# Kernel optimization log

Hardware: AMD Instinct MI355X
Metric: run time of the kernel (lower is better)

Reference implementation:

```python
import jax, jax.numpy as jnp
import numpy as np

B_TREES, NARY, HS, NHEAD, NLVL = 16, 3, 512, 2, 6
EDIM = 352
LN_EPS = 1e-5

def _build_structure():
    # forest of B_TREES perfect ternary trees, depth NLVL; nodes numbered leaves-first, level-major
    off, o = {}, 0
    for l in range(NLVL - 1, -1, -1):
        off[l] = o
        o += B_TREES * 3 ** l
    node_ids = [off[l] + np.arange(B_TREES * 3 ** l) for l in range(NLVL)]
    child_idx = {}
    for l in range(NLVL - 1):
        m = 3 ** l
        t = np.repeat(np.arange(B_TREES), m)
        p = np.tile(np.arange(m), B_TREES)
        base = off[l + 1] + t * (3 ** (l + 1)) + 3 * p
        child_idx[l] = base[:, None] + np.arange(NARY)[None, :]
    return o, node_ids, child_idx

N_NODES, NODE_IDS, CHILD_IDX = _build_structure()

def _ln(x, w, b):
    mu = x.mean(-1, keepdims=True)
    var = x.var(-1, keepdims=True)
    return (x - mu) / jnp.sqrt(var + LN_EPS) * w + b

def _mha(x, wqkv, bqkv, wo, bo):
    # x: [S, B, H]; torch MHA with batch_first=False (seq dim 0, as in reduce_func)
    S, B, H = x.shape
    hd = H // NHEAD
    q, k, v = jnp.split(x @ wqkv.T + bqkv, 3, axis=-1)
    q = q.reshape(S, B, NHEAD, hd)
    k = k.reshape(S, B, NHEAD, hd)
    v = v.reshape(S, B, NHEAD, hd)
    scores = jnp.einsum('sbnd,tbnd->bnst', q, k) / jnp.sqrt(jnp.asarray(hd, x.dtype))
    attn = jax.nn.softmax(scores, axis=-1)
    o = jnp.einsum('bnst,tbnd->sbnd', attn, v).reshape(S, B, H)
    return o @ wo.T + bo

def _transformer(x, qkv_w, qkv_b, out_w, out_b, ln1_w, ln1_b, ff1_w, ff1_b, ff2_w, ff2_b, ln2_w, ln2_b):
    # 2 post-norm TransformerEncoderLayers, relu FF, dropout off (eval)
    for i in range(2):
        x = _ln(x + _mha(x, qkv_w[i], qkv_b[i], out_w[i], out_b[i]), ln1_w[i], ln1_b[i])
        ff = jax.nn.relu(x @ ff1_w[i].T + ff1_b[i]) @ ff2_w[i].T + ff2_b[i]
        x = _ln(x + ff, ln2_w[i], ln2_b[i])
    return x

def _forward(floats, ints):
    (user_emb, poi_emb, cat_emb, coo_emb, time_pos, W_iou, U_iou, b_iou,
     W_f, U_f, b_f, qkv_w, qkv_b, out_w, out_b, ln1_w, ln1_b, ff1_w, ff1_b,
     ff2_w, ff2_b, ln2_w, ln2_b, dec_poi_w, dec_poi_b, dec_cat_w, dec_cat_b,
     dec_coo_w, dec_coo_b) = floats
    user_ids, poi_ids, cat_ids, coo_ids, time_ids, mask = ints
    mi = mask.astype(jnp.int32)
    x = jnp.concatenate([user_emb[user_ids * mi], poi_emb[poi_ids * mi],
                         cat_emb[cat_ids * mi], coo_emb[coo_ids * mi]], axis=1)
    x = x + 0.5 * time_pos[time_ids * mi]
    x = x * mask.astype(x.dtype)[:, None]  # embed_dropout is identity in eval; per-node mask
    h = jnp.zeros((N_NODES, HS), x.dtype)
    c = jnp.zeros((N_NODES, HS), x.dtype)
    # leaves: reduce never fires -> iou stays at W_iou(x) (no b_iou), c = 0
    leaf = NODE_IDS[NLVL - 1]
    i0, o0, u0 = jnp.split(x[leaf] @ W_iou.T, 3, axis=1)
    c_leaf = jax.nn.sigmoid(i0) * jnp.tanh(u0)
    h = h.at[leaf].set(jax.nn.sigmoid(o0) * jnp.tanh(c_leaf))
    c = c.at[leaf].set(c_leaf)
    # topological propagation, bottom-up level frontiers
    for l in range(NLVL - 2, -1, -1):
        idx = NODE_IDS[l]
        ci = CHILD_IDX[l]
        m = idx.shape[0]
        h_ch = h[ci]  # mailbox gather [m, nary, HS]
        c_ch = c[ci]
        xl = x[idx]
        Wx = jnp.tile(xl @ W_f.T, (1, NARY))
        f = jax.nn.sigmoid(Wx + h_ch.reshape(m, NARY * HS) @ U_f.T + jnp.tile(b_f, (1, NARY)))
        h_att = _transformer(h_ch, qkv_w, qkv_b, out_w, out_b, ln1_w, ln1_b,
                             ff1_w, ff1_b, ff2_w, ff2_b, ln2_w, ln2_b)
        iou = xl @ W_iou.T + h_att.reshape(m, NARY * HS) @ U_iou.T + b_iou
        c_red = jnp.sum(f.reshape(m, NARY, HS) * c_ch, axis=1)
        i1, o1, u1 = jnp.split(iou, 3, axis=1)
        c_new = jax.nn.sigmoid(i1) * jnp.tanh(u1) + c_red
        h_new = jax.nn.sigmoid(o1) * jnp.tanh(c_new)
        h = h.at[idx].set(h_new)
        c = c.at[idx].set(c_new)
    # model_dropout identity in eval
    y_poi = h @ dec_poi_w.T + dec_poi_b
    y_cat = h @ dec_cat_w.T + dec_cat_b
    y_coo = h @ dec_coo_w.T + dec_coo_b
    return y_poi, y_cat, y_coo

def setup_inputs():
    key = jax.random.key(0)
    ks = iter(jax.random.split(key, 64))
    def rn(shape, s=0.05):
        return jax.random.normal(next(ks), shape, dtype=jnp.float32) * s
    def ri(shape, hi):
        return jax.random.randint(next(ks), shape, 0, hi, dtype=jnp.int32)
    N = N_NODES
    return dict(
        user_ids=ri([N], 3000), poi_ids=ri([N], 5000), cat_ids=ri([N], 300),
        coo_ids=ri([N], 1024), time_ids=ri([N], 96), mask=ri([N], 2),
        user_emb=rn([3000, 128], 0.02), poi_emb=rn([5000, 128], 0.02),
        cat_emb=rn([300, 32], 0.02), coo_emb=rn([1024, 64], 0.02),
        time_pos=rn([96, EDIM], 0.02),
        W_iou=rn([3 * HS, EDIM]), U_iou=rn([3 * HS, NARY * HS]), b_iou=jnp.zeros((1, 3 * HS)),
        W_f=rn([HS, EDIM]), U_f=rn([NARY * HS, NARY * HS]), b_f=jnp.zeros((1, HS)),
        qkv_w=rn([2, 3 * HS, HS]), qkv_b=jnp.zeros((2, 3 * HS)),
        out_w=rn([2, HS, HS]), out_b=jnp.zeros((2, HS)),
        ln1_w=jnp.ones((2, HS)), ln1_b=jnp.zeros((2, HS)),
        ff1_w=rn([2, HS, HS]), ff1_b=jnp.zeros((2, HS)),
        ff2_w=rn([2, HS, HS]), ff2_b=jnp.zeros((2, HS)),
        ln2_w=jnp.ones((2, HS)), ln2_b=jnp.zeros((2, HS)),
        dec_poi_w=rn([5000, HS]), dec_poi_b=jnp.zeros((5000,)),
        dec_cat_w=rn([300, HS]), dec_cat_b=jnp.zeros((300,)),
        dec_coo_w=rn([1024, HS]), dec_coo_b=jnp.zeros((1024,)),
    )

def reference(user_ids, poi_ids, cat_ids, coo_ids, time_ids, mask,
              user_emb, poi_emb, cat_emb, coo_emb, time_pos,
              W_iou, U_iou, b_iou, W_f, U_f, b_f,
              qkv_w, qkv_b, out_w, out_b, ln1_w, ln1_b, ff1_w, ff1_b,
              ff2_w, ff2_b, ln2_w, ln2_b,
              dec_poi_w, dec_poi_b, dec_cat_w, dec_cat_b, dec_coo_w, dec_coo_b):
    floats = (user_emb, poi_emb, cat_emb, coo_emb, time_pos, W_iou, U_iou, b_iou,
              W_f, U_f, b_f, qkv_w, qkv_b, out_w, out_b, ln1_w, ln1_b, ff1_w, ff1_b,
              ff2_w, ff2_b, ln2_w, ln2_b, dec_poi_w, dec_poi_b, dec_cat_w, dec_cat_b,
              dec_coo_w, dec_coo_b)
    ints = (user_ids, poi_ids, cat_ids, coo_ids, time_ids, mask)
    return _forward(floats, ints)
```

## Files before the change

kernel.cpp:

```cpp
#include <hip/hip_runtime.h>
#include <hip/hip_bf16.h>


namespace {

constexpr int NN = 5824;
constexpr int ED = 352;

typedef __bf16 bf16;
typedef short s16x8 __attribute__((ext_vector_type(8)));
typedef float f32x4 __attribute__((ext_vector_type(4)));

__device__ __forceinline__ float sigmoidf_(float x) { return 1.f / (1.f + expf(-x)); }

__device__ __forceinline__ void gload_lds16(const void* g, void* s) {
  __builtin_amdgcn_global_load_lds(
      (const __attribute__((address_space(1))) unsigned int*)g,
      (__attribute__((address_space(3))) unsigned int*)s, 16, 0, 0);
}

template <int MODE, bool DUAL, bool BPAIR, bool BF32>
__global__ __launch_bounds__(256) void bgemm_k(
    const bf16* __restrict__ A, const bf16* __restrict__ Alo,
    const bf16* __restrict__ Bh_, const bf16* __restrict__ Bl_,
    const float* __restrict__ Bf0, const float* __restrict__ Bf1,
    const float* __restrict__ Bf2,
    void* __restrict__ Cp, bf16* __restrict__ Clo, const float* __restrict__ Cacc,
    const float* __restrict__ bias, const float* __restrict__ bias1,
    const float* __restrict__ bias2, bf16* __restrict__ VTout, int mpad,
    int M, int N, int K, int lda, int ldb, int ldc, float alpha,
    long long sA1, long long sA2, long long sB1, long long sB2,
    long long sC1, long long sC2, int nh) {
  const int bz = blockIdx.z;
  const int b1 = bz / nh, b2 = bz - b1 * nh;
  A += (long long)b1 * sA1 + (long long)b2 * sA2;
  if (DUAL) Alo += (long long)b1 * sA1 + (long long)b2 * sA2;
  if (!BF32) {
    Bh_ += (long long)b1 * sB1 + (long long)b2 * sB2;
    if (BPAIR) Bl_ += (long long)b1 * sB1 + (long long)b2 * sB2;
  }
  const long long coff = (long long)b1 * sC1 + (long long)b2 * sC2;
  const int bm = blockIdx.y * 128, bn = blockIdx.x * 128;
  __shared__ bf16 As[128 * 32];
  __shared__ bf16 Ls[DUAL ? 128 * 32 : 8];
  __shared__ bf16 Bh[128 * 32];
  __shared__ bf16 Bl[BPAIR ? 128 * 32 : 8];
  const int tid = threadIdx.x;
  const int l = tid & 63;
  const int wr = ((tid >> 7) & 1) * 64;
  const int wc = ((tid >> 6) & 1) * 64;
  f32x4 acc[4][4];
#pragma unroll
  for (int i = 0; i < 4; ++i)
#pragma unroll
    for (int j = 0; j < 4; ++j) acc[i][j] = (f32x4){0.f, 0.f, 0.f, 0.f};

  for (int k0 = 0; k0 < K; k0 += 32) {
#pragma unroll
    for (int r = 0; r < 2; ++r) {
      int idx = r * 256 + tid;
      int row = idx >> 2, cs = idx & 3;
      int cg = cs ^ (row & 3);
      int ra = bm + row; if (ra > M - 1) ra = M - 1;
      int rb = bn + row; if (rb > N - 1) rb = N - 1;
      gload_lds16(A + (long long)ra * lda + k0 + cg * 8, As + idx * 8);
      if (DUAL) gload_lds16(Alo + (long long)ra * lda + k0 + cg * 8, Ls + idx * 8);
      if (BF32) {
        const float* src;
        if (rb < 5000)      src = Bf0 + (long long)rb * ldb + k0 + cg * 8;
        else if (rb < 5300) src = Bf1 + (long long)(rb - 5000) * ldb + k0 + cg * 8;
        else                src = Bf2 + (long long)(rb - 5300) * ldb + k0 + cg * 8;
        float4 x = *reinterpret_cast<const float4*>(src);
        float4 y = *reinterpret_cast<const float4*>(src + 4);
        float w[8] = {x.x, x.y, x.z, x.w, y.x, y.y, y.z, y.w};
        bf16 hb_[8], lb_[8];
#pragma unroll
        for (int q = 0; q < 8; ++q) {
          bf16 hq = (bf16)w[q];
          hb_[q] = hq;
          lb_[q] = (bf16)(w[q] - (float)hq);
        }
        *reinterpret_cast<s16x8*>(Bh + idx * 8) = *reinterpret_cast<s16x8*>(hb_);
        *reinterpret_cast<s16x8*>(Bl + idx * 8) = *reinterpret_cast<s16x8*>(lb_);
      } else {
        gload_lds16(Bh_ + (long long)rb * ldb + k0 + cg * 8, Bh + idx * 8);
        if (BPAIR) gload_lds16(Bl_ + (long long)rb * ldb + k0 + cg * 8, Bl + idx * 8);
      }
    }
    __syncthreads();
    s16x8 af[4], al[4], bh[4], bl2[4];
#pragma unroll
    for (int mi = 0; mi < 4; ++mi) {
      int row = wr + mi * 16 + (l & 15);
      int ch = ((l >> 4) ^ row) & 3;
      af[mi] = *reinterpret_cast<const s16x8*>(As + row * 32 + ch * 8);
      if (DUAL) al[mi] = *reinterpret_cast<const s16x8*>(Ls + row * 32 + ch * 8);
    }
#pragma unroll
    for (int ni = 0; ni < 4; ++ni) {
      int row = wc + ni * 16 + (l & 15);
      int ch = ((l >> 4) ^ row) & 3;
      bh[ni] = *reinterpret_cast<const s16x8*>(Bh + row * 32 + ch * 8);
      if (BPAIR) bl2[ni] = *reinterpret_cast<const s16x8*>(Bl + row * 32 + ch * 8);
    }
#pragma unroll
    for (int mi = 0; mi < 4; ++mi)
#pragma unroll
      for (int ni = 0; ni < 4; ++ni) {
        acc[mi][ni] =
            __builtin_amdgcn_mfma_f32_16x16x32_bf16(af[mi], bh[ni], acc[mi][ni], 0, 0, 0);
        if (BPAIR)
          acc[mi][ni] =
              __builtin_amdgcn_mfma_f32_16x16x32_bf16(af[mi], bl2[ni], acc[mi][ni], 0, 0, 0);
        if (DUAL)
          acc[mi][ni] =
              __builtin_amdgcn_mfma_f32_16x16x32_bf16(al[mi], bh[ni], acc[mi][ni], 0, 0, 0);
      }
    __syncthreads();
  }

  const int lc = l & 15, lr4 = (l >> 4) * 4;
#pragma unroll
  for (int mi = 0; mi < 4; ++mi) {
#pragma unroll
    for (int j = 0; j < 4; ++j) {
      int r = bm + wr + mi * 16 + lr4 + j;
      if (MODE != 7 && r >= M) continue;
#pragma unroll
      for (int ni = 0; ni < 4; ++ni) {
        int c = bn + wc + ni * 16 + lc;
        if (c >= N) continue;
        float v = alpha * acc[mi][ni][j];
        if (MODE == 6) {
          v += (c < 5000) ? bias[c] : (c < 5300) ? bias1[c - 5000] : bias2[c - 5300];
        } else if (bias) {
          v += bias[c];
        }
        long long idx = coff + (long long)r * ldc + c;
        if (MODE == 7) {
          if (c >= 1024 && r < 3 * mpad) {
            bf16 pv = (r < M) ? (bf16)v : (bf16)0.f;
            int r3 = r % 3, s = r / 3;
            int hh = (c - 1024) >> 8, n = (c - 1024) & 255;
            VTout[(long long)((r3 * 2 + hh) * 256 + n) * mpad + s] = pv;
          }
          if (r < M) ((bf16*)Cp)[idx] = (bf16)v;
        } else if (MODE == 5) {
          ((float*)Cp)[idx] = v + Cacc[idx];
        } else if (MODE == 0) {
          ((float*)Cp)[idx] = v;
        } else if (MODE == 3) {
          ((bf16*)Cp)[idx] = (bf16)v;
        } else if (MODE == 4) {
          v = fmaxf(v, 0.f);
          bf16 hv = (bf16)v;
          ((bf16*)Cp)[idx] = hv;
          Clo[idx] = (bf16)(v - (float)hv);
        } else {
          float* o0 = (float*)Cp;
          if (c < 5000)      o0[(long long)r * 5000 + c] = v;
          else if (c < 5300) o0[29120000LL + (long long)r * 300 + (c - 5000)] = v;
          else               o0[30867200LL + (long long)r * 1024 + (c - 5300)] = v;
        }
      }
    }
  }
}

static void bgemm(hipStream_t st, int mode, bool dual, bool bpair,
                  const bf16* A, const bf16* Alo, const bf16* Bh, const bf16* Bl,
                  void* Cp, bf16* Clo, const float* Cacc,
                  const float* bias, const float* bias1, const float* bias2,
                  bf16* VTout, int mpad,
                  int M, int N, int K, int lda, int ldb, int ldc, float alpha,
                  int batches = 1, long long sA1 = 0, long long sA2 = 0,
                  long long sB1 = 0, long long sB2 = 0, long long sC1 = 0,
                  long long sC2 = 0, int nh = 1,
                  const float* Bf0 = nullptr, const float* Bf1 = nullptr,
                  const float* Bf2 = nullptr, bool bf32 = false) {
  dim3 g((N + 127) / 128, (M + 127) / 128, batches), b(256);
#define BGL(MD_, DU_, BP_, BFF_)                                                         \
  bgemm_k<MD_, DU_, BP_, BFF_><<<g, b, 0, st>>>(A, Alo, Bh, Bl, Bf0, Bf1, Bf2, Cp, Clo,  \
                                                Cacc, bias, bias1, bias2, VTout, mpad,   \
                                                M, N, K, lda, ldb, ldc, alpha, sA1, sA2, \
                                                sB1, sB2, sC1, sC2, nh)
  if (mode == 0 && !dual && bpair)        BGL(0, false, true, false);
  else if (mode == 0 && dual && bpair)    BGL(0, true, true, false);
  else if (mode == 0 && !dual && !bpair)  BGL(0, false, false, false);
  else if (mode == 3)                     BGL(3, false, false, false);
  else if (mode == 4)                     BGL(4, true, true, false);
  else if (mode == 5)                     BGL(5, true, true, false);
  else if (mode == 6 && !bf32)            BGL(6, true, true, false);
  else if (mode == 6 && bf32)             BGL(6, true, true, true);
  else                                    BGL(7, true, true, false);
#undef BGL
}

struct SegArgs {
  const float* src[8];
  bf16* hi[8];
  bf16* lo[8];
  int start[9];
};
__global__ __launch_bounds__(256) void split_k(SegArgs a, int total8) {
  for (int i = blockIdx.x * 256 + threadIdx.x; i < total8; i += gridDim.x * 256) {
    int s = 0;
    while (i >= a.start[s + 1]) ++s;
    long long off = (long long)(i - a.start[s]) * 8;
    const float4* p = reinterpret_cast<const float4*>(a.src[s] + off);
    float4 x = p[0], y = p[1];
    float w[8] = {x.x, x.y, x.z, x.w, y.x, y.y, y.z, y.w};
    bf16 hb[8], lb[8];
#pragma unroll
    for (int q = 0; q < 8; ++q) {
      bf16 hq = (bf16)w[q];
      hb[q] = hq;
      lb[q] = (bf16)(w[q] - (float)hq);
    }
    *reinterpret_cast<s16x8*>(a.hi[s] + off) = *reinterpret_cast<s16x8*>(hb);
    *reinterpret_cast<s16x8*>(a.lo[s] + off) = *reinterpret_cast<s16x8*>(lb);
  }
}

__global__ __launch_bounds__(256) void embed_k(
    const int* __restrict__ uid, const int* __restrict__ pid, const int* __restrict__ cid,
    const int* __restrict__ gid, const int* __restrict__ tmid, const int* __restrict__ mask,
    const float* __restrict__ ue, const float* __restrict__ pe, const float* __restrict__ ce,
    const float* __restrict__ ge, const float* __restrict__ tp, bf16* __restrict__ xb) {
  int e = blockIdx.x * 256 + threadIdx.x;
  if (e >= NN * ED) return;
  int n = e / ED, j = e - n * ED;
  int mi = mask[n];
  float fm = (float)mi;
  float v;
  if (j < 128)      v = ue[(long long)(uid[n] * mi) * 128 + j];
  else if (j < 256) v = pe[(long long)(pid[n] * mi) * 128 + (j - 128)];
  else if (j < 288) v = ce[(long long)(cid[n] * mi) * 32 + (j - 256)];
  else              v = ge[(long long)(gid[n] * mi) * 64 + (j - 288)];
  v += 0.5f * tp[(long long)(tmid[n] * mi) * ED + j];
  xb[e] = (bf16)(v * fm);
}

__global__ __launch_bounds__(256) void fcred_k(
    const float* __restrict__ wxa, const float* __restrict__ ufh,
    const float* __restrict__ bf_, const float* __restrict__ c, float* __restrict__ cred,
    int m, int cbase, int tl, int woff) {
  int e = blockIdx.x * 256 + threadIdx.x;
  if (e >= m * 512) return;
  int r = e >> 9, d = e & 511;
  float w = wxa[(long long)(woff + r) * 512 + d] + bf_[d];
  int t = r / tl, p = r - t * tl;
  long long cb = (long long)(cbase + t * 3 * tl + 3 * p) * 512 + d;
  long long ub = (long long)r * 1536;
  float acc = 0.f;
#pragma unroll
  for (int k = 0; k < 3; ++k) {
    float f = sigmoidf_(w + ufh[ub + k * 512 + d]);
    acc += f * c[cb + (long long)k * 512];
  }
  cred[e] = acc;
}

__global__ __launch_bounds__(256) void combine_k(
    const float* __restrict__ iou, const float* __restrict__ cred, float* __restrict__ c,
    bf16* __restrict__ hhi, bf16* __restrict__ hlo, int off, int m, int tl3, int tlp,
    bf16* __restrict__ nxthi, bf16* __restrict__ nxtlo) {
  int e = blockIdx.x * 256 + threadIdx.x;
  if (e >= m * 512) return;
  int r = e >> 9, d = e & 511;
  long long b = (long long)r * 1536;
  float iv = iou[b + d], ov = iou[b + 512 + d], uv = iou[b + 1024 + d];
  float cr = cred ? cred[e] : 0.f;
  float cn = sigmoidf_(iv) * tanhf(uv) + cr;
  float hn = sigmoidf_(ov) * tanhf(cn);
  long long o = (long long)(off + r) * 512 + d;
  c[o] = cn;
  bf16 hv = (bf16)hn;
  bf16 lo = (bf16)(hn - (float)hv);
  hhi[o] = hv;
  hlo[o] = lo;
  if (nxthi) {
    int t = r / tl3, q = r - t * tl3;
    int qp = q / 3, slot = q - 3 * qp;
    long long dst = (long long)(t * tlp + qp) * 1536 + slot * 512 + d;
    nxthi[dst] = hv;
    nxtlo[dst] = lo;
  }
}

__global__ __launch_bounds__(256) void ln_k(
    const bf16* __restrict__ ahi, const bf16* __restrict__ alo, const float* __restrict__ b,
    const float* __restrict__ w, const float* __restrict__ bias,
    bf16* __restrict__ ohi, bf16* __restrict__ olo) {
  int r = blockIdx.x, t = threadIdx.x;
  long long base = (long long)r * 512;
  float v0 = (float)ahi[base + t] + (float)alo[base + t] + b[base + t];
  float v1 = (float)ahi[base + 256 + t] + (float)alo[base + 256 + t] + b[base + 256 + t];
  __shared__ float s1[256], s2[256];
  s1[t] = v0 + v1;
  s2[t] = v0 * v0 + v1 * v1;
  __syncthreads();
  for (int s = 128; s > 0; s >>= 1) {
    if (t < s) { s1[t] += s1[t + s]; s2[t] += s2[t + s]; }
    __syncthreads();
  }
  float mu = s1[0] * (1.f / 512.f);
  float var = s2[0] * (1.f / 512.f) - mu * mu;
  float rs = rsqrtf(var + 1e-5f);
  float o0 = (v0 - mu) * rs * w[t] + bias[t];
  float o1 = (v1 - mu) * rs * w[256 + t] + bias[256 + t];
  bf16 h0 = (bf16)o0, h1 = (bf16)o1;
  ohi[base + t] = h0;       olo[base + t] = (bf16)(o0 - (float)h0);
  ohi[base + 256 + t] = h1; olo[base + 256 + t] = (bf16)(o1 - (float)h1);
}

__global__ __launch_bounds__(256) void softmax_pb_k(float* __restrict__ sc, int m, int mpad) {
  long long r = blockIdx.x;
  float* row = sc + r * (long long)m;
  bf16* prow = (bf16*)sc + r * (long long)(2 * m);
  int t = threadIdx.x;
  __shared__ float sh[256];
  float mx = -3.4e38f;
  for (int j = t; j < m; j += 256) mx = fmaxf(mx, row[j]);
  sh[t] = mx;
  __syncthreads();
  for (int s = 128; s > 0; s >>= 1) {
    if (t < s) sh[t] = fmaxf(sh[t], sh[t + s]);
    __syncthreads();
  }
  mx = sh[0];
  __syncthreads();
  float ev[6];
  float sum = 0.f;
  int cnt = 0;
  for (int j = t; j < m; j += 256) {
    float e = expf(row[j] - mx);
    ev[cnt++] = e;
    sum += e;
  }
  sh[t] = sum;
  __syncthreads();
  for (int s = 128; s > 0; s >>= 1) {
    if (t < s) sh[t] += sh[t + s];
    __syncthreads();
  }
  float inv = 1.f / sh[0];
  cnt = 0;
  for (int j = t; j < m; j += 256) prow[j] = (bf16)(ev[cnt++] * inv);
  for (int j = m + t; j < mpad; j += 256) prow[j] = (bf16)0.f;
}

}

extern "C" void kernel_launch(void* const* d_in, const int* in_sizes, int n_in,
                              void* d_out, int out_size, void* d_ws, size_t ws_size,
                              hipStream_t stream) {
  const int* uid  = (const int*)d_in[0];
  const int* pid  = (const int*)d_in[1];
  const int* cid  = (const int*)d_in[2];
  const int* gid  = (const int*)d_in[3];
  const int* tmid = (const int*)d_in[4];
  const int* mask = (const int*)d_in[5];
  const float* ue = (const float*)d_in[6];
  const float* pe = (const float*)d_in[7];
  const float* ce = (const float*)d_in[8];
  const float* ge = (const float*)d_in[9];
  const float* tp = (const float*)d_in[10];
  const float* b_iou = (const float*)d_in[13];
  const float* b_f = (const float*)d_in[16];
  const float* qkv_b = (const float*)d_in[18];
  const float* out_b = (const float*)d_in[20];
  const float* ln1_w = (const float*)d_in[21];
  const float* ln1_b = (const float*)d_in[22];
  const float* ff1_b = (const float*)d_in[24];
  const float* ff2_b = (const float*)d_in[26];
  const float* ln2_w = (const float*)d_in[27];
  const float* ln2_b = (const float*)d_in[28];
  const float* dpw = (const float*)d_in[29];
  const float* dpb = (const float*)d_in[30];
  const float* dcw = (const float*)d_in[31];
  const float* dcb = (const float*)d_in[32];
  const float* dgw = (const float*)d_in[33];
  const float* dgb = (const float*)d_in[34];

  float* ws = (float*)d_ws;
  bf16* Hhi = (bf16*)ws;
  bf16* Hlo = Hhi + 2981888LL;
  float* Cc = ws + 2981888LL;
  bf16* DhiW = (bf16*)(ws + 5963776LL);
  bf16* DloW = DhiW + 3237888LL;
  const bool wsfit = ws_size >= 36806656ULL;

  float* ob = (float*)d_out;
  float* IOUa = ob;
  float* WXa  = ob + 8945664LL;
  float* CRED = ob + 9936896LL;
  bf16* RAhi  = (bf16*)(ob + 10600448LL);
  bf16* RAlo  = RAhi + 1990656LL;
  bf16* RBhi  = (bf16*)(ob + 12591104LL);
  bf16* RBlo  = RBhi + 1990656LL;
  bf16* UP    = (bf16*)(ob + 14581760LL);
  bf16* TE    = (bf16*)(ob + 19300352LL);
  float* TB   = ob + 22446080LL;

  bf16* Uihi = UP;
  bf16* Uilo = UP + 2359296LL;
  bf16* Ufhi = UP + 4718592LL;
  bf16* Uflo = UP + 7077888LL;
  bf16* qkvhi = TE;
  bf16* qkvlo = TE + 1572864LL;
  bf16* outhi = TE + 3145728LL;
  bf16* outlo = TE + 3670016LL;
  bf16* ff1hi = TE + 4194304LL;
  bf16* ff1lo = TE + 4718592LL;
  bf16* ff2hi = TE + 5242880LL;
  bf16* ff2lo = TE + 5767168LL;

  float* SC   = TB;
  float* PQ   = TB + 10077696LL;
  bf16* VT    = (bf16*)(TB + 13063680LL);
  bf16* Xb    = (bf16*)TB;
  bf16* WP    = (bf16*)(TB + 1025024LL);
  bf16* Wihi  = WP;
  bf16* Wilo  = WP + 540672LL;
  bf16* Wfhi  = WP + 1081344LL;
  bf16* Wflo  = WP + 1261568LL;

  float* UFH  = PQ;
  bf16* QKVb  = (bf16*)PQ;
  bf16* ATTOb = (bf16*)PQ;
  float* XB   = TB;
  bf16* XChi  = (bf16*)(TB + 1990656LL);
  bf16* XClo  = (bf16*)(TB + 2985984LL);

  {
    SegArgs a{};
    const int n8[8] = {294912, 294912, 196608, 65536, 65536, 65536, 67584, 22528};
    a.src[0] = (const float*)d_in[12]; a.hi[0] = Uihi;  a.lo[0] = Uilo;
    a.src[1] = (const float*)d_in[15]; a.hi[1] = Ufhi;  a.lo[1] = Uflo;
    a.src[2] = (const float*)d_in[17]; a.hi[2] = qkvhi; a.lo[2] = qkvlo;
    a.src[3] = (const float*)d_in[19]; a.hi[3] = outhi; a.lo[3] = outlo;
    a.src[4] = (const float*)d_in[23]; a.hi[4] = ff1hi; a.lo[4] = ff1lo;
    a.src[5] = (const float*)d_in[25]; a.hi[5] = ff2hi; a.lo[5] = ff2lo;
    a.src[6] = (const float*)d_in[11]; a.hi[6] = Wihi;  a.lo[6] = Wilo;
    a.src[7] = (const float*)d_in[14]; a.hi[7] = Wfhi;  a.lo[7] = Wflo;
    a.start[0] = 0;
    for (int i = 0; i < 8; ++i) a.start[i + 1] = a.start[i] + n8[i];
    int total8 = a.start[8];
    int blocks = (total8 + 255) / 256; if (blocks > 4096) blocks = 4096;
    split_k<<<blocks, 256, 0, stream>>>(a, total8);
    if (wsfit) {
      SegArgs d{};
      const int dn8[3] = {320000, 19200, 65536};
      d.src[0] = dpw; d.hi[0] = DhiW;             d.lo[0] = DloW;
      d.src[1] = dcw; d.hi[1] = DhiW + 2560000LL; d.lo[1] = DloW + 2560000LL;
      d.src[2] = dgw; d.hi[2] = DhiW + 2713600LL; d.lo[2] = DloW + 2713600LL;
      d.start[0] = 0;
      for (int i = 0; i < 3; ++i) d.start[i + 1] = d.start[i] + dn8[i];
      for (int i = 3; i < 8; ++i) d.start[i + 1] = d.start[3];
      int dt8 = d.start[3];
      int db = (dt8 + 255) / 256; if (db > 4096) db = 4096;
      split_k<<<db, 256, 0, stream>>>(d, dt8);
    }
  }

  embed_k<<<(NN * ED + 255) / 256, 256, 0, stream>>>(uid, pid, cid, gid, tmid, mask,
                                                     ue, pe, ce, ge, tp, Xb);

  bgemm(stream, 0, false, true, Xb, nullptr, Wihi, Wilo, IOUa, nullptr, nullptr,
        nullptr, nullptr, nullptr, nullptr, 0, NN, 1536, 352, 352, 352, 1536, 1.f);
  bgemm(stream, 0, false, true, Xb + 3888LL * ED, nullptr, Wfhi, Wflo, WXa, nullptr,
        nullptr, nullptr, nullptr, nullptr, nullptr, 0, 1936, 512, 352, 352, 352, 512, 1.f);

  combine_k<<<(3888 * 512 + 255) / 256, 256, 0, stream>>>(
      IOUa, nullptr, Cc, Hhi, Hlo, 0, 3888, 243, 81, RAhi, RAlo);

  static const int OFFL[6] = {5808, 5760, 5616, 5184, 3888, 0};
  int tl = 81;
  for (int l = 4; l >= 0; --l, tl /= 3) {
    int m = 16 * tl;
    int off = OFFL[l];
    int cbase = OFFL[l + 1];
    int T = 3 * m;
    int mpad = (m + 31) & ~31;

    bgemm(stream, 0, true, true, RAhi, RAlo, Ufhi, Uflo, UFH, nullptr, nullptr,
          nullptr, nullptr, nullptr, nullptr, 0, m, 1536, 1536, 1536, 1536, 1536, 1.f);
    fcred_k<<<(m * 512 + 255) / 256, 256, 0, stream>>>(WXa, UFH, b_f, Cc, CRED,
                                                       m, cbase, tl, off - 3888);

    bf16 *curhi = RAhi, *curlo = RAlo, *nxthi = RBhi, *nxtlo = RBlo;
    for (int i = 0; i < 2; ++i) {
      bgemm(stream, 7, true, true, curhi, curlo, qkvhi + (long long)i * 786432,
            qkvlo + (long long)i * 786432, QKVb, nullptr, nullptr,
            qkv_b + i * 1536, nullptr, nullptr, VT, mpad,
            T, 1536, 512, 512, 512, 1536, 1.f);
      bgemm(stream, 0, false, false, QKVb, nullptr, QKVb + 512, nullptr, SC, nullptr,
            nullptr, nullptr, nullptr, nullptr, nullptr, 0,
            m, m, 256, 4608, 4608, m, 0.0625f,
            6, 1536, 256, 1536, 256, 2LL * m * m, (long long)m * m, 2);
      softmax_pb_k<<<6 * m, 256, 0, stream>>>(SC, m, mpad);
      bgemm(stream, 3, false, false, (bf16*)SC, nullptr, VT, nullptr, ATTOb, nullptr,
            nullptr, nullptr, nullptr, nullptr, nullptr, 0,
            m, 256, mpad, 2 * m, mpad, 1536, 1.f,
            6, 4LL * m * m, 2LL * m * m, 2LL * 256 * mpad, 256LL * mpad, 512, 256, 2);
      bgemm(stream, 0, false, true, ATTOb, nullptr, outhi + (long long)i * 262144,
            outlo + (long long)i * 262144, XB, nullptr, nullptr,
            out_b + i * 512, nullptr, nullptr, nullptr, 0,
            T, 512, 512, 512, 512, 512, 1.f);
      ln_k<<<T, 256, 0, stream>>>(curhi, curlo, XB, ln1_w + i * 512, ln1_b + i * 512,
                                  nxthi, nxtlo);
      bgemm(stream, 4, true, true, nxthi, nxtlo, ff1hi + (long long)i * 262144,
            ff1lo + (long long)i * 262144, XChi, XClo, nullptr,
            ff1_b + i * 512, nullptr, nullptr, nullptr, 0,
            T, 512, 512, 512, 512, 512, 1.f);
      bgemm(stream, 0, true, true, XChi, XClo, ff2hi + (long long)i * 262144,
            ff2lo + (long long)i * 262144, XB, nullptr, nullptr,
            ff2_b + i * 512, nullptr, nullptr, nullptr, 0,
            T, 512, 512, 512, 512, 512, 1.f);
      ln_k<<<T, 256, 0, stream>>>(nxthi, nxtlo, XB, ln2_w + i * 512, ln2_b + i * 512,
                                  curhi, curlo);
    }

    bgemm(stream, 5, true, true, curhi, curlo, Uihi, Uilo,
          IOUa + (long long)off * 1536, nullptr, IOUa + (long long)off * 1536,
          b_iou, nullptr, nullptr, nullptr, 0, m, 1536, 1536, 1536, 1536, 1536, 1.f);
    combine_k<<<(m * 512 + 255) / 256, 256, 0, stream>>>(
        IOUa + (long long)off * 1536, CRED, Cc, Hhi, Hlo, off, m, tl, tl / 3,
        l > 0 ? RAhi : nullptr, l > 0 ? RAlo : nullptr);
  }

  if (wsfit) {
    bgemm(stream, 6, true, true, Hhi, Hlo, DhiW, DloW, ob, nullptr, nullptr,
          dpb, dcb, dgb, nullptr, 0, NN, 6324, 512, 512, 512, 0, 1.f);
  } else {
    bgemm(stream, 6, true, true, Hhi, Hlo, nullptr, nullptr, ob, nullptr, nullptr,
          dpb, dcb, dgb, nullptr, 0, NN, 6324, 512, 512, 512, 0, 1.f,
          1, 0, 0, 0, 0, 0, 0, 1, dpw, dcw, dgw, true);
  }
}
```

Measured before the change: 2.667 ms.

## Double-buffer LDS tiles in small-grid GEMMs and swizzle mode-6 blocks across XCDs

Adds a templated PIPE path to the bf16 MFMA GEMM that double-buffers the A/B LDS tiles, so global→LDS loads for the next K-slice are issued before computing the current one, with one barrier per iteration. It is selected only when the grid has at most 256 blocks and the B operand is not converted from fp32, which targets under-occupied launches where load latency is exposed. Mode-6 (decoder) launches also remap block indices so consecutive tiles land on the same XCD, to improve L2 reuse. The cost is doubled LDS use (possibly lower occupancy) and more template instantiations.

```diff
diff --git a/kernel.cpp b/kernel.cpp
--- a/kernel.cpp
+++ b/kernel.cpp
@@ -19,7 +19,7 @@
       (__attribute__((address_space(3))) unsigned int*)s, 16, 0, 0);
 }
 
-template <int MODE, bool DUAL, bool BPAIR, bool BF32>
+template <int MODE, bool DUAL, bool BPAIR, bool BF32, bool PIPE>
 __global__ __launch_bounds__(256) void bgemm_k(
     const bf16* __restrict__ A, const bf16* __restrict__ Alo,
     const bf16* __restrict__ Bh_, const bf16* __restrict__ Bl_,
@@ -40,11 +40,24 @@
     if (BPAIR) Bl_ += (long long)b1 * sB1 + (long long)b2 * sB2;
   }
   const long long coff = (long long)b1 * sC1 + (long long)b2 * sC2;
-  const int bm = blockIdx.y * 128, bn = blockIdx.x * 128;
-  __shared__ bf16 As[128 * 32];
-  __shared__ bf16 Ls[DUAL ? 128 * 32 : 8];
-  __shared__ bf16 Bh[128 * 32];
-  __shared__ bf16 Bl[BPAIR ? 128 * 32 : 8];
+
+  int bxx = blockIdx.x, byy = blockIdx.y;
+  if (MODE == 6) {
+    int nwg = gridDim.x * gridDim.y;
+    int orig = byy * gridDim.x + bxx;
+    int q = nwg >> 3, r = nwg & 7;
+    int xcd = orig & 7, idx = orig >> 3;
+    int wg = (xcd < r ? xcd * (q + 1) : r * (q + 1) + (xcd - r) * q) + idx;
+    bxx = wg % gridDim.x;
+    byy = wg / gridDim.x;
+  }
+  const int bm = byy * 128, bn = bxx * 128;
+
+  constexpr int NSTG = PIPE ? 2 : 1;
+  __shared__ bf16 As[NSTG][128 * 32];
+  __shared__ bf16 Ls[DUAL ? NSTG : 1][DUAL ? 128 * 32 : 8];
+  __shared__ bf16 Bh[NSTG][128 * 32];
+  __shared__ bf16 Bl[BPAIR ? NSTG : 1][BPAIR ? 128 * 32 : 8];
   const int tid = threadIdx.x;
   const int l = tid & 63;
   const int wr = ((tid >> 7) & 1) * 64;
@@ -55,7 +68,7 @@
 #pragma unroll
     for (int j = 0; j < 4; ++j) acc[i][j] = (f32x4){0.f, 0.f, 0.f, 0.f};
 
-  for (int k0 = 0; k0 < K; k0 += 32) {
+  auto STAGE = [&](int st, int k0) {
 #pragma unroll
     for (int r = 0; r < 2; ++r) {
       int idx = r * 256 + tid;
@@ -63,8 +76,8 @@
       int cg = cs ^ (row & 3);
       int ra = bm + row; if (ra > M - 1) ra = M - 1;
       int rb = bn + row; if (rb > N - 1) rb = N - 1;
-      gload_lds16(A + (long long)ra * lda + k0 + cg * 8, As + idx * 8);
-      if (DUAL) gload_lds16(Alo + (long long)ra * lda + k0 + cg * 8, Ls + idx * 8);
+      gload_lds16(A + (long long)ra * lda + k0 + cg * 8, &As[st][idx * 8]);
+      if (DUAL) gload_lds16(Alo + (long long)ra * lda + k0 + cg * 8, &Ls[st][idx * 8]);
       if (BF32) {
         const float* src;
         if (rb < 5000)      src = Bf0 + (long long)rb * ldb + k0 + cg * 8;
@@ -80,43 +93,66 @@
           hb_[q] = hq;
           lb_[q] = (bf16)(w[q] - (float)hq);
         }
-        *reinterpret_cast<s16x8*>(Bh + idx * 8) = *reinterpret_cast<s16x8*>(hb_);
-        *reinterpret_cast<s16x8*>(Bl + idx * 8) = *reinterpret_cast<s16x8*>(lb_);
+        *reinterpret_cast<s16x8*>(&Bh[st][idx * 8]) = *reinterpret_cast<s16x8*>(hb_);
+        *reinterpret_cast<s16x8*>(&Bl[st][idx * 8]) = *reinterpret_cast<s16x8*>(lb_);
       } else {
-        gload_lds16(Bh_ + (long long)rb * ldb + k0 + cg * 8, Bh + idx * 8);
-        if (BPAIR) gload_lds16(Bl_ + (long long)rb * ldb + k0 + cg * 8, Bl + idx * 8);
+        gload_lds16(Bh_ + (long long)rb * ldb + k0 + cg * 8, &Bh[st][idx * 8]);
+        if (BPAIR) gload_lds16(Bl_ + (long long)rb * ldb + k0 + cg * 8, &Bl[st][idx * 8]);
       }
     }
-    __syncthreads();
-    s16x8 af[4], al[4], bh[4], bl2[4];
+  };
+
+  auto COMPUTE = [&](int st) {
+    s16x8 af[4], al[4], bh4[4], bl4[4];
 #pragma unroll
     for (int mi = 0; mi < 4; ++mi) {
       int row = wr + mi * 16 + (l & 15);
       int ch = ((l >> 4) ^ row) & 3;
-      af[mi] = *reinterpret_cast<const s16x8*>(As + row * 32 + ch * 8);
-      if (DUAL) al[mi] = *reinterpret_cast<const s16x8*>(Ls + row * 32 + ch * 8);
+      af[mi] = *reinterpret_cast<const s16x8*>(&As[st][row * 32 + ch * 8]);
+      if (DUAL) al[mi] = *reinterpret_cast<const s16x8*>(&Ls[st][row * 32 + ch * 8]);
     }
 #pragma unroll
     for (int ni = 0; ni < 4; ++ni) {
       int row = wc + ni * 16 + (l & 15);
       int ch = ((l >> 4) ^ row) & 3;
-      bh[ni] = *reinterpret_cast<const s16x8*>(Bh + row * 32 + ch * 8);
-      if (BPAIR) bl2[ni] = *reinterpret_cast<const s16x8*>(Bl + row * 32 + ch * 8);
+      bh4[ni] = *reinterpret_cast<const s16x8*>(&Bh[st][row * 32 + ch * 8]);
+      if (BPAIR) bl4[ni] = *reinterpret_cast<const s16x8*>(&Bl[st][row * 32 + ch * 8]);
     }
 #pragma unroll
     for (int mi = 0; mi < 4; ++mi)
 #pragma unroll
       for (int ni = 0; ni < 4; ++ni) {
         acc[mi][ni] =
-            __builtin_amdgcn_mfma_f32_16x16x32_bf16(af[mi], bh[ni], acc[mi][ni], 0, 0, 0);
+            __builtin_amdgcn_mfma_f32_16x16x32_bf16(af[mi], bh4[ni], acc[mi][ni], 0, 0, 0);
         if (BPAIR)
           acc[mi][ni] =
-              __builtin_amdgcn_mfma_f32_16x16x32_bf16(af[mi], bl2[ni], acc[mi][ni], 0, 0, 0);
+              __builtin_amdgcn_mfma_f32_16x16x32_bf16(af[mi], bl4[ni], acc[mi][ni], 0, 0, 0);
         if (DUAL)
           acc[mi][ni] =
-              __builtin_amdgcn_mfma_f32_16x16x32_bf16(al[mi], bh[ni], acc[mi][ni], 0, 0, 0);
+              __builtin_amdgcn_mfma_f32_16x16x32_bf16(al[mi], bh4[ni], acc[mi][ni], 0, 0, 0);
       }
-    __syncthreads();
+  };
+
+  if (!PIPE) {
+    for (int k0 = 0; k0 < K; k0 += 32) {
+      STAGE(0, k0);
+      __syncthreads();
+      COMPUTE(0);
+      __syncthreads();
+    }
+  } else {
+    STAGE(0, 0);
+    asm volatile("s_waitcnt vmcnt(0)" ::: "memory");
+    __builtin_amdgcn_s_barrier();
+    int cur = 0;
+    for (int k0 = 0; k0 < K; k0 += 32) {
+      if (k0 + 32 < K) STAGE(cur ^ 1, k0 + 32);
+      COMPUTE(cur);
+      asm volatile("s_waitcnt vmcnt(0)" ::: "memory");
+      __builtin_amdgcn_sched_barrier(0);
+      __builtin_amdgcn_s_barrier();
+      cur ^= 1;
+    }
   }
 
   const int lc = l & 15, lr4 = (l >> 4) * 4;
@@ -179,20 +215,25 @@
                   const float* Bf0 = nullptr, const float* Bf1 = nullptr,
                   const float* Bf2 = nullptr, bool bf32 = false) {
   dim3 g((N + 127) / 128, (M + 127) / 128, batches), b(256);
-#define BGL(MD_, DU_, BP_, BFF_)                                                         \
-  bgemm_k<MD_, DU_, BP_, BFF_><<<g, b, 0, st>>>(A, Alo, Bh, Bl, Bf0, Bf1, Bf2, Cp, Clo,  \
-                                                Cacc, bias, bias1, bias2, VTout, mpad,   \
-                                                M, N, K, lda, ldb, ldc, alpha, sA1, sA2, \
-                                                sB1, sB2, sC1, sC2, nh)
-  if (mode == 0 && !dual && bpair)        BGL(0, false, true, false);
-  else if (mode == 0 && dual && bpair)    BGL(0, true, true, false);
-  else if (mode == 0 && !dual && !bpair)  BGL(0, false, false, false);
-  else if (mode == 3)                     BGL(3, false, false, false);
-  else if (mode == 4)                     BGL(4, true, true, false);
-  else if (mode == 5)                     BGL(5, true, true, false);
-  else if (mode == 6 && !bf32)            BGL(6, true, true, false);
-  else if (mode == 6 && bf32)             BGL(6, true, true, true);
-  else                                    BGL(7, true, true, false);
+  long long nblocks = (long long)g.x * g.y * g.z;
+  const bool pipe = (!bf32) && nblocks <= 256;
+#define BGL(MD_, DU_, BP_, BFF_, PP_)                                                    \
+  bgemm_k<MD_, DU_, BP_, BFF_, PP_><<<g, b, 0, st>>>(                                    \
+      A, Alo, Bh, Bl, Bf0, Bf1, Bf2, Cp, Clo, Cacc, bias, bias1, bias2, VTout, mpad,     \
+      M, N, K, lda, ldb, ldc, alpha, sA1, sA2, sB1, sB2, sC1, sC2, nh)
+#define BGL2(MD_, DU_, BP_)                                                              \
+  do { if (pipe) BGL(MD_, DU_, BP_, false, true); else BGL(MD_, DU_, BP_, false, false); \
+  } while (0)
+  if (mode == 0 && !dual && bpair)        BGL2(0, false, true);
+  else if (mode == 0 && dual && bpair)    BGL2(0, true, true);
+  else if (mode == 0 && !dual && !bpair)  BGL2(0, false, false);
+  else if (mode == 3)                     BGL2(3, false, false);
+  else if (mode == 4)                     BGL2(4, true, true);
+  else if (mode == 5)                     BGL2(5, true, true);
+  else if (mode == 6 && !bf32)            BGL(6, true, true, false, false);
+  else if (mode == 6 && bf32)             BGL(6, true, true, true, false);
+  else                                    BGL2(7, true, true);
+#undef BGL2
 #undef BGL
 }
 
```

Result: no change. 2.654 ms (-0.5%).
